# Performance work log

Measured on AMD Instinct MI355X. Metric: run time of the kernel, lower is better.

The kernel has to match this reference:

```python
import jax, jax.numpy as jnp
import numpy as np

H, D = 4, 32            # heads, head_dim
HID = H * D             # hidden_channels = 128
L = 2                   # num_layers
N = (100000, 50000)     # (n_session, n_item)
E = 200000              # edges per relation
ETYPES = ((0, 1), (1, 0), (1, 1))  # (src_type, dst_type) per relation


def _seg_softmax(alpha, dst, num_dst):
    # alpha: [E, H]; softmax over edges sharing the same dst node
    amax = jax.ops.segment_max(alpha, dst, num_segments=num_dst)
    amax = jnp.where(jnp.isfinite(amax), amax, 0.0)
    ex = jnp.exp(alpha - amax[dst])
    s = jax.ops.segment_sum(ex, dst, num_segments=num_dst)
    return ex / (s[dst] + 1e-16)


def _hgt_conv(xs, Wk, bk, Wq, bq, Wv, bv, Wa, ba, skip, a_rel, m_rel, p_rel, edges):
    # per-node-type k/q/v projections, reshaped to [N_t, H, D]
    k = [(x @ Wk[t] + bk[t]).reshape(-1, H, D) for t, x in enumerate(xs)]
    q = [(x @ Wq[t] + bq[t]).reshape(-1, H, D) for t, x in enumerate(xs)]
    v = [(x @ Wv[t] + bv[t]).reshape(-1, H, D) for t, x in enumerate(xs)]
    agg = [jnp.zeros((N[t], H, D), xs[0].dtype) for t in range(len(xs))]
    scale = 1.0 / jnp.sqrt(jnp.asarray(D, xs[0].dtype))
    for r, ((st, dt), (src, dst)) in enumerate(zip(ETYPES, edges)):
        kr = jnp.einsum('nhd,hde->nhe', k[st], a_rel[r])  # relation-specific key
        vr = jnp.einsum('nhd,hde->nhe', v[st], m_rel[r])  # relation-specific value
        alpha = jnp.einsum('ehd,ehd->eh', q[dt][dst], kr[src]) * p_rel[r] * scale
        alpha = _seg_softmax(alpha, dst, N[dt])
        msg = vr[src] * alpha[..., None]                  # [E, H, D]
        agg[dt] = agg[dt] + jax.ops.segment_sum(msg, dst, num_segments=N[dt])
    out = []
    for t in range(len(xs)):
        o = jax.nn.gelu(agg[t].reshape(N[t], HID), approximate=False) @ Wa[t] + ba[t]
        a = jax.nn.sigmoid(skip[t])
        out.append(a * o + (1.0 - a) * xs[t])
    return out


def setup_inputs() -> dict:
    key = jax.random.key(0)
    ks = jax.random.split(key, 16)
    f_in = 128
    s = 1.0 / np.sqrt(HID)
    return {
        'x0': jax.random.normal(ks[0], (N[0], f_in), jnp.float32),
        'x1': jax.random.normal(ks[1], (N[1], f_in), jnp.float32),
        'src0': jax.random.randint(ks[2], (E,), 0, N[0], jnp.int32),
        'dst0': jax.random.randint(ks[3], (E,), 0, N[1], jnp.int32),
        'src1': jax.random.randint(ks[4], (E,), 0, N[1], jnp.int32),
        'dst1': jax.random.randint(ks[5], (E,), 0, N[0], jnp.int32),
        'src2': jax.random.randint(ks[6], (E,), 0, N[1], jnp.int32),
        'dst2': jax.random.randint(ks[7], (E,), 0, N[1], jnp.int32),
        'W_in': jax.random.normal(ks[8], (2, f_in, HID), jnp.float32) / np.sqrt(f_in),
        'b_in': jnp.zeros((2, HID), jnp.float32),
        'Wk': jax.random.normal(ks[9], (L, 2, HID, HID), jnp.float32) * s,
        'bk': jnp.zeros((L, 2, HID), jnp.float32),
        'Wq': jax.random.normal(ks[10], (L, 2, HID, HID), jnp.float32) * s,
        'bq': jnp.zeros((L, 2, HID), jnp.float32),
        'Wv': jax.random.normal(ks[11], (L, 2, HID, HID), jnp.float32) * s,
        'bv': jnp.zeros((L, 2, HID), jnp.float32),
        'Wa': jax.random.normal(ks[12], (L, 2, HID, HID), jnp.float32) * s,
        'ba': jnp.zeros((L, 2, HID), jnp.float32),
        'skip': jnp.ones((L, 2), jnp.float32),
        'a_rel': jax.random.normal(ks[13], (L, 3, H, D, D), jnp.float32) / np.sqrt(D),
        'm_rel': jax.random.normal(ks[14], (L, 3, H, D, D), jnp.float32) / np.sqrt(D),
        'p_rel': jnp.ones((L, 3, H), jnp.float32),
    }


def reference(x0, x1, src0, dst0, src1, dst1, src2, dst2,
              W_in, b_in, Wk, bk, Wq, bq, Wv, bv, Wa, ba, skip,
              a_rel, m_rel, p_rel):
    edges = ((src0, dst0), (src1, dst1), (src2, dst2))
    h = [jax.nn.relu(x0 @ W_in[0] + b_in[0]),
         jax.nn.relu(x1 @ W_in[1] + b_in[1])]
    outs = [h]
    for l in range(L):
        h = _hgt_conv(h, Wk[l], bk[l], Wq[l], bq[l], Wv[l], bv[l],
                      Wa[l], ba[l], skip[l], a_rel[l], m_rel[l], p_rel[l], edges)
        outs.append(h)
    y0 = jnp.concatenate([o[0] for o in outs], axis=1)  # [N0, HID*(L+1)]
    y1 = jnp.concatenate([o[1] for o in outs], axis=1)  # [N1, HID*(L+1)]
    return (y0, y1)
```

## Files before the change

kernel.cpp:

```cpp
#include <hip/hip_runtime.h>
#include <math.h>


#define HID 128
#define OLD 384

typedef __attribute__((ext_vector_type(8))) short short8;
typedef __attribute__((ext_vector_type(4))) float f32x4;

__device__ __forceinline__ unsigned short f2b(float f) {
    unsigned u = __float_as_uint(f);
    u += 0x7fffu + ((u >> 16) & 1u);
    return (unsigned short)(u >> 16);
}
__device__ __forceinline__ unsigned pk2(float a, float b) {
    return (unsigned)f2b(a) | ((unsigned)f2b(b) << 16);
}
__device__ __forceinline__ float blo(unsigned u) { return __uint_as_float(u << 16); }
__device__ __forceinline__ float bhi(unsigned u) { return __uint_as_float(u & 0xffff0000u); }
__device__ __forceinline__ float gelu_f(float x) {
    return 0.5f * x * (1.0f + erff(x * 0.70710678118654752f));
}

template <int AFP32>
__device__ __forceinline__ void load_bfrag(short8 (&d)[4], const void* Aptr,
                                           int lda, int node, int kq)
{
    if (AFP32) {
        const float* ar = (const float*)Aptr + (size_t)node * lda;
#pragma unroll
        for (int kt = 0; kt < 4; ++kt) {
            float4 v0 = *(const float4*)(ar + kt * 32 + kq * 8);
            float4 v1 = *(const float4*)(ar + kt * 32 + kq * 8 + 4);
            short8 t;
            t[0] = (short)f2b(v0.x); t[1] = (short)f2b(v0.y);
            t[2] = (short)f2b(v0.z); t[3] = (short)f2b(v0.w);
            t[4] = (short)f2b(v1.x); t[5] = (short)f2b(v1.y);
            t[6] = (short)f2b(v1.z); t[7] = (short)f2b(v1.w);
            d[kt] = t;
        }
    } else {
        const unsigned short* ar = (const unsigned short*)Aptr + (size_t)node * lda;
#pragma unroll
        for (int kt = 0; kt < 4; ++kt)
            d[kt] = *(const short8*)(ar + kt * 32 + kq * 8);
    }
}

template <int AFP32, int EPI, int BRES>
__device__ __forceinline__ void gemm_body(
    int yb,
    const void* __restrict__ A0, const void* __restrict__ A1, int lda,
    const unsigned short* __restrict__ Wp, const float* __restrict__ biasP,
    int wblk0, int wblk1, int nct0, int nct1,
    unsigned short* __restrict__ Cb0, unsigned short* __restrict__ Cb1,
    int ldcb0, int ldcb1,
    float* __restrict__ Cf0, float* __restrict__ Cf1, int ldcf,
    const unsigned short* __restrict__ Hb0, const unsigned short* __restrict__ Hb1,
    const float* __restrict__ skipP,
    int M0, int M1, int yb0)
{
    const int tid  = threadIdx.x;
    const int wid  = tid >> 6;
    const int lane = tid & 63;
    const int ow = (wid >> 1) * 64;
    const int nw = (wid & 1) * 64;
    const int lm = lane & 15;
    const int kq = lane >> 4;

    const int t  = (yb >= yb0) ? 1 : 0;
    const int r0 = (t ? (yb - yb0) : yb) * 128;
    const int M    = t ? M1 : M0;
    const int nct  = t ? nct1 : nct0;
    const int wblk = t ? wblk1 : wblk0;
    const void* Aptr = t ? A1 : A0;
    unsigned short* Cb = t ? Cb1 : Cb0;
    const int ldcb = t ? ldcb1 : ldcb0;
    float* Cf = t ? Cf1 : Cf0;
    const unsigned short* Hb = t ? Hb1 : Hb0;

    short8 bres[4][4];
    if (BRES) {
#pragma unroll
        for (int ni = 0; ni < 4; ++ni) {
            int node = r0 + nw + ni * 16 + lm;
            node = (node < M) ? node : (M - 1);
            load_bfrag<AFP32>(bres[ni], Aptr, lda, node, kq);
        }
    }

    float aa = 0.f, ab = 0.f;
    if (EPI == 2) {
        const float sv = skipP[t];
        aa = 1.0f / (1.0f + __expf(-sv));
        ab = 1.0f - aa;
    }

    for (int ct = 0; ct < nct; ++ct) {
        const unsigned short* wbase = Wp + (size_t)(wblk + ct) * 16384;
        short8 wf[4][4];
#pragma unroll
        for (int mi = 0; mi < 4; ++mi) {
            const int mt = (ow >> 4) + mi;
#pragma unroll
            for (int kt = 0; kt < 4; ++kt)
                wf[mi][kt] = *(const short8*)(wbase + (((mt * 4 + kt) * 64 + lane) << 3));
        }

        f32x4 acc[4][4];
#pragma unroll
        for (int ni = 0; ni < 4; ++ni)
#pragma unroll
            for (int mi = 0; mi < 4; ++mi)
                acc[ni][mi] = (f32x4){0.f, 0.f, 0.f, 0.f};

#pragma unroll
        for (int ni = 0; ni < 4; ++ni) {
            if (BRES) {
#pragma unroll
                for (int kt = 0; kt < 4; ++kt)
#pragma unroll
                    for (int mi = 0; mi < 4; ++mi)
                        acc[ni][mi] = __builtin_amdgcn_mfma_f32_16x16x32_bf16(
                            wf[mi][kt], bres[ni][kt], acc[ni][mi], 0, 0, 0);
            } else {
                int node = r0 + nw + ni * 16 + lm;
                node = (node < M) ? node : (M - 1);
                short8 bl[4];
                load_bfrag<AFP32>(bl, Aptr, lda, node, kq);
#pragma unroll
                for (int kt = 0; kt < 4; ++kt)
#pragma unroll
                    for (int mi = 0; mi < 4; ++mi)
                        acc[ni][mi] = __builtin_amdgcn_mfma_f32_16x16x32_bf16(
                            wf[mi][kt], bl[kt], acc[ni][mi], 0, 0, 0);
            }
        }

        float4 b4[4];
#pragma unroll
        for (int mi = 0; mi < 4; ++mi)
            b4[mi] = *(const float4*)(biasP + (wblk + ct) * 128 + ow + mi * 16 + kq * 4);

#pragma unroll
        for (int ni = 0; ni < 4; ++ni) {
            const int node = r0 + nw + ni * 16 + lm;
            if (node >= M) continue;
#pragma unroll
            for (int mi = 0; mi < 4; ++mi) {
                const int oc = ow + mi * 16 + kq * 4;
                float v0 = acc[ni][mi][0] + b4[mi].x;
                float v1 = acc[ni][mi][1] + b4[mi].y;
                float v2 = acc[ni][mi][2] + b4[mi].z;
                float v3 = acc[ni][mi][3] + b4[mi].w;
                if (EPI == 1) {
                    v0 = fmaxf(v0, 0.f); v1 = fmaxf(v1, 0.f);
                    v2 = fmaxf(v2, 0.f); v3 = fmaxf(v3, 0.f);
                }
                if (EPI == 2) {
                    uint2 hp = *(const uint2*)(Hb + (size_t)node * 128 + oc);
                    v0 = aa * v0 + ab * blo(hp.x);
                    v1 = aa * v1 + ab * bhi(hp.x);
                    v2 = aa * v2 + ab * blo(hp.y);
                    v3 = aa * v3 + ab * bhi(hp.y);
                }
                if (EPI != 0) {
                    *(float4*)(Cf + (size_t)node * ldcf + oc) =
                        make_float4(v0, v1, v2, v3);
                    *(uint2*)(Cb + (size_t)node * 128 + oc) =
                        make_uint2(pk2(v0, v1), pk2(v2, v3));
                } else {
                    *(uint2*)(Cb + (size_t)node * ldcb + ct * 128 + oc) =
                        make_uint2(pk2(v0, v1), pk2(v2, v3));
                }
            }
        }
    }
}

template <int AFP32, int EPI, int BRES>
__global__ __launch_bounds__(256) void mfma_gemm(
    const void* __restrict__ A0, const void* __restrict__ A1, int lda,
    const unsigned short* __restrict__ Wp, const float* __restrict__ biasP,
    int wblk0, int wblk1, int nct0, int nct1,
    unsigned short* __restrict__ Cb0, unsigned short* __restrict__ Cb1,
    int ldcb0, int ldcb1,
    float* __restrict__ Cf0, float* __restrict__ Cf1, int ldcf,
    const unsigned short* __restrict__ Hb0, const unsigned short* __restrict__ Hb1,
    const float* __restrict__ skipP,
    int M0, int M1, int yb0)
{
    gemm_body<AFP32, EPI, BRES>(blockIdx.x, A0, A1, lda, Wp, biasP,
        wblk0, wblk1, nct0, nct1, Cb0, Cb1, ldcb0, ldcb1,
        Cf0, Cf1, ldcf, Hb0, Hb1, skipP, M0, M1, yb0);
}

__device__ __forceinline__ void attn_loop(
    const unsigned short* __restrict__ kv, size_t ldkv, int kof, int vof,
    const int* __restrict__ rowptr, const int* __restrict__ esrc,
    int n, int lane, float q0, float q1,
    float& o0, float& o1)
{
    const int p0 = rowptr[n], p1 = rowptr[n + 1];
    float m = -INFINITY, l = 0.f, a0 = 0.f, a1 = 0.f;
    if (p0 < p1) {
        const int s0 = esrc[p0];
        const unsigned short* sp = kv + (size_t)s0 * ldkv + 2 * lane;
        unsigned kp = *(const unsigned*)(sp + kof);
        unsigned vp = *(const unsigned*)(sp + vof);
        for (int p = p0; p < p1; ++p) {
            const unsigned kc = kp, vc = vp;
            if (p + 1 < p1) {
                const int sn = esrc[p + 1];
                const unsigned short* spn = kv + (size_t)sn * ldkv + 2 * lane;
                kp = *(const unsigned*)(spn + kof);
                vp = *(const unsigned*)(spn + vof);
            }
            float al = q0 * blo(kc) + q1 * bhi(kc);
            al += __shfl_xor(al, 1, 64);
            al += __shfl_xor(al, 2, 64);
            al += __shfl_xor(al, 4, 64);
            al += __shfl_xor(al, 8, 64);
            const float nm  = fmaxf(m, al);
            const float scl = __expf(m - nm);
            const float w   = __expf(al - nm);
            l  = l * scl + w;
            a0 = a0 * scl + w * blo(vc);
            a1 = a1 * scl + w * bhi(vc);
            m  = nm;
        }
    }
    const float inv = 1.0f / (l + 1e-16f);
    o0 = a0 * inv;
    o1 = a1 * inv;
}

__global__ __launch_bounds__(256) void hgt_attn(
    const unsigned short* __restrict__ qkv0,
    const unsigned short* __restrict__ qkv1,
    const int* __restrict__ rp1, const int* __restrict__ es1,
    const int* __restrict__ rp0, const int* __restrict__ es0,
    const int* __restrict__ rp2, const int* __restrict__ es2,
    unsigned short* __restrict__ agg0, unsigned short* __restrict__ agg1,
    int N0, int N1, int nb1)
{
    const int wid = threadIdx.x >> 6, lane = threadIdx.x & 63;
    const int b = blockIdx.x;
    if (b < nb1) {
        const int n = b * 4 + wid;
        if (n >= N1) return;
        const unsigned qp = *(const unsigned*)(qkv1 + (size_t)n * 640 + 2 * lane);
        const float q0 = blo(qp), q1 = bhi(qp);
        float x0, x1, y0, y1;
        attn_loop(qkv0, 384, 128, 256, rp0, es0, n, lane, q0, q1, x0, x1);
        attn_loop(qkv1, 640, 384, 512, rp2, es2, n, lane, q0, q1, y0, y1);
        *(unsigned*)(agg1 + (size_t)n * 128 + 2 * lane) =
            pk2(gelu_f(x0 + y0), gelu_f(x1 + y1));
    } else {
        const int n = (b - nb1) * 4 + wid;
        if (n >= N0) return;
        const unsigned qp = *(const unsigned*)(qkv0 + (size_t)n * 384 + 2 * lane);
        float o0, o1;
        attn_loop(qkv1, 640, 128, 256, rp1, es1, n, lane, blo(qp), bhi(qp), o0, o1);
        *(unsigned*)(agg0 + (size_t)n * 128 + 2 * lane) = pk2(gelu_f(o0), gelu_f(o1));
    }
}

__global__ void hgt_prep(
    const float* __restrict__ W_in, const float* __restrict__ b_in,
    const float* __restrict__ Wk, const float* __restrict__ bk,
    const float* __restrict__ Wq, const float* __restrict__ bq,
    const float* __restrict__ Wv, const float* __restrict__ bv,
    const float* __restrict__ Wa, const float* __restrict__ ba,
    const float* __restrict__ a_rel, const float* __restrict__ m_rel,
    const float* __restrict__ p_rel,
    unsigned short* __restrict__ Bp, float* __restrict__ bp,
    const int* __restrict__ d0, const int* __restrict__ d1,
    const int* __restrict__ d2, int E, int N0v, int N1v,
    int* __restrict__ deg)
{
    if (blockIdx.y < 3) {
        const int r = blockIdx.y;
        const int e = blockIdx.x * 256 + threadIdx.x;
        if (e >= E) return;
        const int* dd = (r == 0) ? d0 : (r == 1) ? d1 : d2;
        const int doff = (r == 0) ? 0 : (r == 1) ? N1v : (N1v + N0v);
        atomicAdd(&deg[doff + dd[e]], 1);
        return;
    }
    const int bid = blockIdx.x;
    if (bid >= 22) return;

    const float* Wsrc = nullptr;
    const float* bsrc = nullptr;
    int l = -1, r = 0, kv = 0;
    if      (bid <  2) { Wsrc = W_in + (size_t)bid * 16384; bsrc = b_in + bid * 128; }
    else if (bid == 2) { Wsrc = Wq;                bsrc = bq; }
    else if (bid <= 4) { l = 0; r = 0; kv = bid - 3; }
    else if (bid == 5) { Wsrc = Wq + 16384;        bsrc = bq + 128; }
    else if (bid <= 7) { l = 0; r = 1; kv = bid - 6; }
    else if (bid <= 9) { l = 0; r = 2; kv = bid - 8; }
    else if (bid == 10){ Wsrc = Wa;                bsrc = ba; }
    else if (bid == 11){ Wsrc = Wa + 16384;        bsrc = ba + 128; }
    else if (bid == 12){ Wsrc = Wq + 2 * 16384;    bsrc = bq + 256; }
    else if (bid <= 14){ l = 1; r = 0; kv = bid - 13; }
    else if (bid == 15){ Wsrc = Wq + 3 * 16384;    bsrc = bq + 384; }
    else if (bid <= 17){ l = 1; r = 1; kv = bid - 16; }
    else if (bid <= 19){ l = 1; r = 2; kv = bid - 18; }
    else if (bid == 20){ Wsrc = Wa + 2 * 16384;    bsrc = ba + 256; }
    else               { Wsrc = Wa + 3 * 16384;    bsrc = ba + 384; }

    const bool iscw = (l >= 0);
    const float* rel = nullptr;
    if (iscw) {
        const int st = (r == 0) ? 0 : 1;
        Wsrc = (kv ? Wv : Wk) + (size_t)(l * 2 + st) * 16384;
        bsrc = (kv ? bv : bk) + (l * 2 + st) * 128;
        rel  = (kv ? m_rel : a_rel) + (size_t)(l * 3 + r) * 4096;
    }

    for (int i = threadIdx.x; i < 16384; i += 256) {
        const int mt = i >> 11, kt = (i >> 9) & 3, ln = (i >> 3) & 63, j = i & 7;
        const int m = mt * 16 + (ln & 15);
        const int k = kt * 32 + (ln >> 4) * 8 + j;
        float v;
        if (!iscw) {
            v = Wsrc[k * 128 + m];
        } else {
            const int h = m >> 5, e = m & 31;
            const float fac = kv ? 1.0f
                : p_rel[(l * 3 + r) * 4 + h] * 0.17677669529663687f;
            const float* wr = Wsrc + (size_t)k * 128 + h * 32;
            const float* rc = rel + h * 1024 + e;
            float s = 0.f;
#pragma unroll
            for (int d = 0; d < 32; ++d) s = fmaf(wr[d], rc[d * 32], s);
            v = s * fac;
        }
        Bp[(size_t)bid * 16384 + i] = f2b(v);
    }
    if (threadIdx.x < 128) {
        const int n = threadIdx.x;
        float v;
        if (!iscw) {
            v = bsrc[n];
        } else {
            const int h = n >> 5, e = n & 31;
            const float fac = kv ? 1.0f
                : p_rel[(l * 3 + r) * 4 + h] * 0.17677669529663687f;
            const float* rc = rel + h * 1024 + e;
            float s = 0.f;
#pragma unroll
            for (int d = 0; d < 32; ++d) s = fmaf(bsrc[h * 32 + d], rc[d * 32], s);
            v = s * fac;
        }
        bp[bid * 128 + n] = v;
    }
}

__global__ void hgt_scan1(const int* __restrict__ deg, int* __restrict__ rowptr,
                          int* __restrict__ bsums, int N0v, int N1v)
{
    const int r = blockIdx.y;
    const int Nd = (r == 1) ? N0v : N1v;
    const int n  = Nd + 1;
    if (blockIdx.x * 512 >= n) return;
    const int doff = (r == 0) ? 0 : (r == 1) ? N1v : (N1v + N0v);
    const int roff = (r == 0) ? 0 : (r == 1) ? (N1v + 1) : (N1v + N0v + 2);
    __shared__ int s[512];
    const int tid = threadIdx.x;
    const int i = blockIdx.x * 512 + tid;
    const int v = (i < Nd) ? deg[doff + i] : 0;
    s[tid] = v;
    __syncthreads();
    for (int off = 1; off < 512; off <<= 1) {
        const int t = (tid >= off) ? s[tid - off] : 0;
        __syncthreads();
        s[tid] += t;
        __syncthreads();
    }
    if (i < n) rowptr[roff + i] = s[tid] - v;
    if (tid == 511) bsums[r * 256 + blockIdx.x] = s[511];
}

__global__ void hgt_scan23(int* __restrict__ rowptr, const int* __restrict__ bsums,
                           int N0v, int N1v)
{
    const int r = blockIdx.y;
    const int n = ((r == 1) ? N0v : N1v) + 1;
    if (blockIdx.x * 512 >= n) return;
    const int roff = (r == 0) ? 0 : (r == 1) ? (N1v + 1) : (N1v + N0v + 2);
    const int tid = threadIdx.x;
    int v = (tid < (int)blockIdx.x) ? bsums[r * 256 + tid] : 0;
#pragma unroll
    for (int o = 1; o < 64; o <<= 1) v += __shfl_xor(v, o, 64);
    __shared__ int ws[8];
    if ((tid & 63) == 0) ws[tid >> 6] = v;
    __syncthreads();
    int base = 0;
#pragma unroll
    for (int k = 0; k < 8; ++k) base += ws[k];
    const int i = blockIdx.x * 512 + tid;
    if (i < n) rowptr[roff + i] += base;
}

__global__ __launch_bounds__(256) void hgt_fill_inproj(
    const int* __restrict__ s0, const int* __restrict__ d0,
    const int* __restrict__ s1, const int* __restrict__ d1,
    const int* __restrict__ s2, const int* __restrict__ d2,
    int E, int N0v, int N1v,
    const int* __restrict__ rowptr, int* __restrict__ cnt,
    int* __restrict__ esrc, int eb,
    const float* __restrict__ x0, const float* __restrict__ x1,
    const unsigned short* __restrict__ Wp, const float* __restrict__ biasP,
    unsigned short* __restrict__ hb0, unsigned short* __restrict__ hb1,
    float* __restrict__ outp, int nGemm, int yb0)
{
    const int b = blockIdx.x;
    if (b < nGemm) {
        gemm_body<1, 1, 0>(b, x0, x1, 128, Wp, biasP, 0, 1, 1, 1,
                           hb0, hb1, 128, 128,
                           outp, outp + (size_t)N0v * OLD, OLD,
                           nullptr, nullptr, nullptr, N0v, N1v, yb0);
        return;
    }
    const int bb = b - nGemm;
    const int r = bb / eb;
    const int e = (bb - r * eb) * 256 + (int)threadIdx.x;
    if (e >= E) return;
    const int* ss = (r == 0) ? s0 : (r == 1) ? s1 : s2;
    const int* dd = (r == 0) ? d0 : (r == 1) ? d1 : d2;
    const int doff = (r == 0) ? 0 : (r == 1) ? N1v : (N1v + N0v);
    const int roff = (r == 0) ? 0 : (r == 1) ? (N1v + 1) : (N1v + N0v + 2);
    const int d = dd[e];
    const int pos = atomicAdd(&cnt[doff + d], 1);
    esrc[(size_t)r * E + rowptr[roff + d] + pos] = ss[e];
}

extern "C" void kernel_launch(void* const* d_in, const int* in_sizes, int n_in,
                              void* d_out, int out_size, void* d_ws, size_t ws_size,
                              hipStream_t stream)
{
    const float* x0  = (const float*)d_in[0];
    const float* x1  = (const float*)d_in[1];
    const int* src0 = (const int*)d_in[2];
    const int* dst0 = (const int*)d_in[3];
    const int* src1 = (const int*)d_in[4];
    const int* dst1 = (const int*)d_in[5];
    const int* src2 = (const int*)d_in[6];
    const int* dst2 = (const int*)d_in[7];
    const float* W_in = (const float*)d_in[8];
    const float* b_in = (const float*)d_in[9];
    const float* Wk = (const float*)d_in[10];
    const float* bk = (const float*)d_in[11];
    const float* Wq = (const float*)d_in[12];
    const float* bq = (const float*)d_in[13];
    const float* Wv = (const float*)d_in[14];
    const float* bv = (const float*)d_in[15];
    const float* Wa = (const float*)d_in[16];
    const float* ba = (const float*)d_in[17];
    const float* skip = (const float*)d_in[18];
    const float* a_rel = (const float*)d_in[19];
    const float* m_rel = (const float*)d_in[20];
    const float* p_rel = (const float*)d_in[21];

    const int N0 = in_sizes[0] / HID;
    const int N1 = in_sizes[1] / HID;
    const int E  = in_sizes[2];
    float* out = (float*)d_out;
    (void)n_in; (void)out_size; (void)ws_size;

    char* p = (char*)d_ws;
    auto carve = [&](size_t bytes) -> char* {
        char* q = p;
        p += (bytes + 255) & ~(size_t)255;
        return q;
    };
    unsigned short* hbf  = (unsigned short*)carve((size_t)(N0 + N1) * 128 * 2);
    unsigned short* qkv0 = (unsigned short*)carve((size_t)N0 * 384 * 2);
    unsigned short* qkv1 = (unsigned short*)carve((size_t)N1 * 640 * 2);
    unsigned short* agg  = (unsigned short*)carve((size_t)(N0 + N1) * 128 * 2);
    unsigned short* packW = (unsigned short*)carve((size_t)22 * 16384 * 2);
    float* packb = (float*)carve((size_t)22 * 128 * 4);
    int* rowptr = (int*)carve((size_t)(N0 + 2 * N1 + 3) * 4);
    int* esrc   = (int*)carve((size_t)3 * E * 4);
    char* zbase = carve(0);
    int* deg   = (int*)carve((size_t)(N0 + 2 * N1) * 4);
    int* cnt   = (int*)carve((size_t)(N0 + 2 * N1) * 4);
    int* bsums = (int*)carve(3 * 256 * 4);
    const size_t zbytes = (size_t)((char*)(bsums + 3 * 256) - zbase);

    unsigned short* hbf1 = hbf + (size_t)N0 * 128;
    unsigned short* agg0 = agg;
    unsigned short* agg1 = agg + (size_t)N0 * 128;
    const int* rp0 = rowptr;
    const int* rp1 = rowptr + (N1 + 1);
    const int* rp2 = rowptr + (N1 + N0 + 2);
    const int* es0 = esrc;
    const int* es1 = esrc + (size_t)E;
    const int* es2 = esrc + (size_t)2 * E;

    const int eb  = (E + 255) / 256;
    const int nbx = (N0 + 1 + 511) / 512;
    const int mbN0 = (N0 + 127) / 128;
    const int mbN1 = (N1 + 127) / 128;
    const int nGemm = mbN0 + mbN1;

    hipMemsetAsync(zbase, 0, zbytes, stream);

    hgt_prep<<<dim3(eb, 4), 256, 0, stream>>>(
        W_in, b_in, Wk, bk, Wq, bq, Wv, bv, Wa, ba,
        a_rel, m_rel, p_rel, packW, packb,
        dst0, dst1, dst2, E, N0, N1, deg);

    hgt_scan1 <<<dim3(nbx, 3), 512, 0, stream>>>(deg, rowptr, bsums, N0, N1);
    hgt_scan23<<<dim3(nbx, 3), 512, 0, stream>>>(rowptr, bsums, N0, N1);

    hgt_fill_inproj<<<nGemm + 3 * eb, 256, 0, stream>>>(
        src0, dst0, src1, dst1, src2, dst2, E, N0, N1,
        rowptr, cnt, (int*)esrc, eb,
        x0, x1, packW, packb, hbf, hbf1, out, nGemm, mbN0);

    for (int l = 0; l < 2; ++l) {
        const int qkv0_blk = l ? 12 : 2;
        const int qkv1_blk = l ? 15 : 5;
        const int out0_blk = l ? 20 : 10;
        const int out1_blk = l ? 21 : 11;

        mfma_gemm<0, 0, 1><<<nGemm, 256, 0, stream>>>(
            hbf1, hbf, 128, packW, packb,
            qkv1_blk, qkv0_blk, 5, 3,
            qkv1, qkv0, 640, 384,
            nullptr, nullptr, 0,
            nullptr, nullptr, nullptr,
            N1, N0, mbN1);

        const int nb1 = (N1 + 3) / 4;
        const int nb0 = (N0 + 3) / 4;
        hgt_attn<<<nb1 + nb0, 256, 0, stream>>>(
            qkv0, qkv1, rp1, es1, rp0, es0, rp2, es2,
            agg0, agg1, N0, N1, nb1);

        mfma_gemm<0, 2, 0><<<nGemm, 256, 0, stream>>>(
            agg0, agg1, 128, packW, packb,
            out0_blk, out1_blk, 1, 1,
            hbf, hbf1, 128, 128,
            out + (size_t)(l + 1) * 128,
            out + (size_t)N0 * OLD + (size_t)(l + 1) * 128, OLD,
            hbf, hbf1, skip + l * 2, N0, N1, mbN0);
    }
}
```

Measured before the change: 872.1 us.

## Split each node's edges across four lane groups with 16-byte loads in attention

The attention kernel now gives each wave four 16-lane groups. Each group walks every fourth incoming edge, and each lane handles 8 channels through uint4 loads. Per-group online-softmax states (max, sum, accumulators) are merged at the end with cross-lane shuffles. The aim is more edge-level parallelism per node and fewer shuffle reductions per edge, which should hide gather latency. The cost is extra registers, a final merge step, and wasted iterations when a node's degree is not a multiple of four.

```diff
diff --git a/kernel.cpp b/kernel.cpp
--- a/kernel.cpp
+++ b/kernel.cpp
@@ -195,44 +195,73 @@
         Cf0, Cf1, ldcf, Hb0, Hb1, skipP, M0, M1, yb0);
 }
 
-__device__ __forceinline__ void attn_loop(
-    const unsigned short* __restrict__ kv, size_t ldkv, int kof, int vof,
+__device__ __forceinline__ void attn_loop4(
+    const unsigned short* __restrict__ kv, int ldkv, int koff, int voff,
     const int* __restrict__ rowptr, const int* __restrict__ esrc,
-    int n, int lane, float q0, float q1,
-    float& o0, float& o1)
+    int n, int g, const float* qf,
+    float* a, float& lO)
 {
     const int p0 = rowptr[n], p1 = rowptr[n + 1];
-    float m = -INFINITY, l = 0.f, a0 = 0.f, a1 = 0.f;
+    float m = -1e30f, l = 0.f;
+#pragma unroll
+    for (int j = 0; j < 8; ++j) a[j] = 0.f;
     if (p0 < p1) {
-        const int s0 = esrc[p0];
-        const unsigned short* sp = kv + (size_t)s0 * ldkv + 2 * lane;
-        unsigned kp = *(const unsigned*)(sp + kof);
-        unsigned vp = *(const unsigned*)(sp + vof);
-        for (int p = p0; p < p1; ++p) {
-            const unsigned kc = kp, vc = vp;
-            if (p + 1 < p1) {
-                const int sn = esrc[p + 1];
-                const unsigned short* spn = kv + (size_t)sn * ldkv + 2 * lane;
-                kp = *(const unsigned*)(spn + kof);
-                vp = *(const unsigned*)(spn + vof);
+        const int nit = (p1 - p0 + 3) >> 2;
+        int p = p0 + g;
+        bool valid = (p < p1);
+        {
+            const int s = esrc[valid ? p : (p1 - 1)];
+            const unsigned short* rp = kv + (size_t)s * ldkv;
+            uint4 kp = *(const uint4*)(rp + koff);
+            uint4 vp = *(const uint4*)(rp + voff);
+            for (int it = 0; it < nit; ++it) {
+                const uint4 kc = kp, vc = vp;
+                const bool vld = valid;
+                p += 4;
+                if (it + 1 < nit) {
+                    valid = (p < p1);
+                    const int s2 = esrc[valid ? p : (p1 - 1)];
+                    const unsigned short* r2 = kv + (size_t)s2 * ldkv;
+                    kp = *(const uint4*)(r2 + koff);
+                    vp = *(const uint4*)(r2 + voff);
+                }
+                float al = qf[0] * blo(kc.x) + qf[1] * bhi(kc.x);
+                al += qf[2] * blo(kc.y) + qf[3] * bhi(kc.y);
+                al += qf[4] * blo(kc.z) + qf[5] * bhi(kc.z);
+                al += qf[6] * blo(kc.w) + qf[7] * bhi(kc.w);
+                al += __shfl_xor(al, 1, 64);
+                al += __shfl_xor(al, 2, 64);
+                al = vld ? al : -2e30f;
+                const float nm  = fmaxf(m, al);
+                const float scl = __expf(m - nm);
+                const float w   = __expf(al - nm);
+                l = l * scl + w;
+                a[0] = a[0] * scl + w * blo(vc.x);
+                a[1] = a[1] * scl + w * bhi(vc.x);
+                a[2] = a[2] * scl + w * blo(vc.y);
+                a[3] = a[3] * scl + w * bhi(vc.y);
+                a[4] = a[4] * scl + w * blo(vc.z);
+                a[5] = a[5] * scl + w * bhi(vc.z);
+                a[6] = a[6] * scl + w * blo(vc.w);
+                a[7] = a[7] * scl + w * bhi(vc.w);
+                m = nm;
             }
-            float al = q0 * blo(kc) + q1 * bhi(kc);
-            al += __shfl_xor(al, 1, 64);
-            al += __shfl_xor(al, 2, 64);
-            al += __shfl_xor(al, 4, 64);
-            al += __shfl_xor(al, 8, 64);
-            const float nm  = fmaxf(m, al);
-            const float scl = __expf(m - nm);
-            const float w   = __expf(al - nm);
-            l  = l * scl + w;
-            a0 = a0 * scl + w * blo(vc);
-            a1 = a1 * scl + w * bhi(vc);
-            m  = nm;
-        }
-    }
-    const float inv = 1.0f / (l + 1e-16f);
-    o0 = a0 * inv;
-    o1 = a1 * inv;
+        }
+    }
+    float mo = fmaxf(m, __shfl_xor(m, 16, 64));
+    const float M = fmaxf(mo, __shfl_xor(mo, 32, 64));
+    const float sc = __expf(m - M);
+    l *= sc;
+#pragma unroll
+    for (int j = 0; j < 8; ++j) a[j] *= sc;
+    l += __shfl_xor(l, 16, 64);
+    l += __shfl_xor(l, 32, 64);
+#pragma unroll
+    for (int j = 0; j < 8; ++j) {
+        a[j] += __shfl_xor(a[j], 16, 64);
+        a[j] += __shfl_xor(a[j], 32, 64);
+    }
+    lO = l;
 }
 
 __global__ __launch_bounds__(256) void hgt_attn(
@@ -245,24 +274,50 @@
     int N0, int N1, int nb1)
 {
     const int wid = threadIdx.x >> 6, lane = threadIdx.x & 63;
+    const int u = lane & 15, g = lane >> 4;
+    const int uo = u * 8;
     const int b = blockIdx.x;
+    float qf[8];
     if (b < nb1) {
         const int n = b * 4 + wid;
         if (n >= N1) return;
-        const unsigned qp = *(const unsigned*)(qkv1 + (size_t)n * 640 + 2 * lane);
-        const float q0 = blo(qp), q1 = bhi(qp);
-        float x0, x1, y0, y1;
-        attn_loop(qkv0, 384, 128, 256, rp0, es0, n, lane, q0, q1, x0, x1);
-        attn_loop(qkv1, 640, 384, 512, rp2, es2, n, lane, q0, q1, y0, y1);
-        *(unsigned*)(agg1 + (size_t)n * 128 + 2 * lane) =
-            pk2(gelu_f(x0 + y0), gelu_f(x1 + y1));
+        const uint4 qp = *(const uint4*)(qkv1 + (size_t)n * 640 + uo);
+        qf[0] = blo(qp.x); qf[1] = bhi(qp.x);
+        qf[2] = blo(qp.y); qf[3] = bhi(qp.y);
+        qf[4] = blo(qp.z); qf[5] = bhi(qp.z);
+        qf[6] = blo(qp.w); qf[7] = bhi(qp.w);
+        float ax[8], ay[8], lx, ly;
+        attn_loop4(qkv0, 384, 128 + uo, 256 + uo, rp0, es0, n, g, qf, ax, lx);
+        attn_loop4(qkv1, 640, 384 + uo, 512 + uo, rp2, es2, n, g, qf, ay, ly);
+        if (g == 0) {
+            const float ix = 1.0f / (lx + 1e-16f);
+            const float iy = 1.0f / (ly + 1e-16f);
+            uint4 o;
+            o.x = pk2(gelu_f(ax[0] * ix + ay[0] * iy), gelu_f(ax[1] * ix + ay[1] * iy));
+            o.y = pk2(gelu_f(ax[2] * ix + ay[2] * iy), gelu_f(ax[3] * ix + ay[3] * iy));
+            o.z = pk2(gelu_f(ax[4] * ix + ay[4] * iy), gelu_f(ax[5] * ix + ay[5] * iy));
+            o.w = pk2(gelu_f(ax[6] * ix + ay[6] * iy), gelu_f(ax[7] * ix + ay[7] * iy));
+            *(uint4*)(agg1 + (size_t)n * 128 + uo) = o;
+        }
     } else {
         const int n = (b - nb1) * 4 + wid;
         if (n >= N0) return;
-        const unsigned qp = *(const unsigned*)(qkv0 + (size_t)n * 384 + 2 * lane);
-        float o0, o1;
-        attn_loop(qkv1, 640, 128, 256, rp1, es1, n, lane, blo(qp), bhi(qp), o0, o1);
-        *(unsigned*)(agg0 + (size_t)n * 128 + 2 * lane) = pk2(gelu_f(o0), gelu_f(o1));
+        const uint4 qp = *(const uint4*)(qkv0 + (size_t)n * 384 + uo);
+        qf[0] = blo(qp.x); qf[1] = bhi(qp.x);
+        qf[2] = blo(qp.y); qf[3] = bhi(qp.y);
+        qf[4] = blo(qp.z); qf[5] = bhi(qp.z);
+        qf[6] = blo(qp.w); qf[7] = bhi(qp.w);
+        float av[8], lv;
+        attn_loop4(qkv1, 640, 128 + uo, 256 + uo, rp1, es1, n, g, qf, av, lv);
+        if (g == 0) {
+            const float inv = 1.0f / (lv + 1e-16f);
+            uint4 o;
+            o.x = pk2(gelu_f(av[0] * inv), gelu_f(av[1] * inv));
+            o.y = pk2(gelu_f(av[2] * inv), gelu_f(av[3] * inv));
+            o.z = pk2(gelu_f(av[4] * inv), gelu_f(av[5] * inv));
+            o.w = pk2(gelu_f(av[6] * inv), gelu_f(av[7] * inv));
+            *(uint4*)(agg0 + (size_t)n * 128 + uo) = o;
+        }
     }
 }
 
```

New measurement: 871.2 us. About the same (-0.1%).
